# Kernel optimization log

Measured on AMD Instinct MI355X. Metric: run time of the kernel, lower is better.

The kernel has to match this reference:

```python
import jax, jax.numpy as jnp
import numpy as np
from math import sqrt

I = 1024  # input_size
H = 1024  # hidden_size
B = 4096  # batch


def setup_inputs() -> dict:
    key = jax.random.key(0)
    ks = jax.random.split(key, 12)
    a = 1.0 / sqrt(H)
    u = lambda k, shape: jax.random.uniform(k, shape, jnp.float32, -a, a)
    return {
        "x": jax.random.normal(ks[0], (B, I), jnp.float32),
        "hx": jax.random.normal(ks[1], (B, H), jnp.float32),
        "cx": jax.random.normal(ks[2], (B, H), jnp.float32),
        "weight_ih": u(ks[3], (4 * H, I)),
        "weight_hh": u(ks[4], (4 * H, H)),
        "bias_ih": u(ks[5], (4 * H,)),
        "bias_hh": u(ks[6], (4 * H,)),
        "W_peephole_i": u(ks[7], (H, H)),
        "W_peephole_f": u(ks[8], (H, H)),
        "W_peephole_o": u(ks[9], (H, H)),
    }


def reference(x, hx, cx, weight_ih, weight_hh, bias_ih, bias_hh,
              W_peephole_i, W_peephole_f, W_peephole_o):
    # gates: [B, 4H]
    gates = x @ weight_ih.T + bias_ih + hx @ weight_hh.T + bias_hh
    ingate, forgetgate, cellgate, outgate = jnp.split(gates, 4, axis=1)
    # F.linear(cx, W * eye) == cx * diag(W)  (diagonal peephole)
    ingate = jax.nn.sigmoid(ingate + cx * jnp.diagonal(W_peephole_i))
    forgetgate = jax.nn.sigmoid(forgetgate + cx * jnp.diagonal(W_peephole_f))
    cellgate = jnp.tanh(cellgate)
    cy = forgetgate * cx + ingate * cellgate
    # NOTE: original code reuses W_peephole_f for the output gate (faithful to source)
    outgate = jax.nn.sigmoid(outgate + cy * jnp.diagonal(W_peephole_f))
    hy = outgate * jnp.tanh(cy)
    return (hy, cy)
```

## Files before the change

kernel.cpp:

```cpp
#include <hip/hip_runtime.h>
#include <cstdint>


namespace {

constexpr int H   = 1024;
constexpr int K2  = 2048;
constexpr int BSZ = 4096;
constexpr size_t OUT_CY = (size_t)BSZ * H;

typedef __attribute__((ext_vector_type(8))) short bf16x8;
typedef __attribute__((ext_vector_type(4))) float f32x4;
typedef __attribute__((ext_vector_type(8))) unsigned short u16x8;

__device__ __forceinline__ unsigned short f2bf(float f) {
  union { float f; uint32_t u; } v; v.f = f;
  uint32_t u = v.u;
  u += 0x7FFFu + ((u >> 16) & 1u);
  return (unsigned short)(u >> 16);
}

__device__ __forceinline__ float sigm(float x) {
  return 1.0f / (1.0f + __expf(-x));
}
__device__ __forceinline__ float tanh_fast(float x) {
  return 1.0f - 2.0f / (1.0f + __expf(2.0f * x));
}

__device__ __forceinline__ void gload_lds16(const void* g, void* l) {
  __builtin_amdgcn_global_load_lds(
      (const __attribute__((address_space(1))) void*)g,
      (__attribute__((address_space(3))) void*)l, 16, 0, 0);
}

}

__global__ __launch_bounds__(256) void cast_kernel(
    const float* __restrict__ x, const float* __restrict__ hx,
    const float* __restrict__ wih, const float* __restrict__ whh,
    unsigned short* __restrict__ A, unsigned short* __restrict__ W) {
  int b = blockIdx.x;
  bool isW = b >= 4096;
  int t = (isW ? b - 4096 : b) * 256 + threadIdx.x;
  int idx = t * 8;
  int n = idx >> 11;
  int k = idx & 2047;
  const float* s0 = isW ? wih : x;
  const float* s1 = isW ? whh : hx;
  const float* src = (k < H) ? (s0 + (size_t)n * H + k)
                             : (s1 + (size_t)n * H + (k - H));
  float4 v0 = *(const float4*)src;
  float4 v1 = *(const float4*)(src + 4);
  u16x8 o;
  o[0] = f2bf(v0.x); o[1] = f2bf(v0.y); o[2] = f2bf(v0.z); o[3] = f2bf(v0.w);
  o[4] = f2bf(v1.x); o[5] = f2bf(v1.y); o[6] = f2bf(v1.z); o[7] = f2bf(v1.w);
  if (isW) {
    int g = n >> 10, hh = n & 1023;
    int np = ((hh >> 4) << 6) + (g << 4) + (hh & 15);
    *(u16x8*)(W + (size_t)np * K2 + k) = o;
  } else {
    *(u16x8*)(A + (size_t)idx) = o;
  }
}

__global__ __launch_bounds__(512, 2) void lstm_fused_gemm(
    const unsigned short* __restrict__ A,
    const unsigned short* __restrict__ W,
    const float* __restrict__ cx,
    const float* __restrict__ bias_ih, const float* __restrict__ bias_hh,
    const float* __restrict__ Wpi, const float* __restrict__ Wpf,
    float* __restrict__ out) {
  __shared__ __align__(16) unsigned short lds[2 * 32768];

  const int tid  = threadIdx.x;
  const int lane = tid & 63;
  const int wave = tid >> 6;
  const int wm   = wave >> 2;
  const int wn   = wave & 3;
  const int m0 = blockIdx.x * 256;
  const int w0 = blockIdx.y * 256;

  const int srow   = tid >> 3;
  const int schunk = ((tid & 7) ^ (srow & 7)) << 3;

  const int col  = lane & 15;
  const int quad = lane >> 4;

  const unsigned short* Asrc = A + (size_t)(m0 + srow) * K2 + schunk;
  const unsigned short* Wsrc = W + (size_t)(w0 + srow) * K2 + schunk;
  const int ldsdst = wave * 512;

  f32x4 acc[8][4];
#pragma unroll
  for (int i = 0; i < 8; ++i)
#pragma unroll
    for (int j = 0; j < 4; ++j)
      acc[i][j] = (f32x4){0.f, 0.f, 0.f, 0.f};

  auto stA = [&](int kt, int buf, int p) {
    gload_lds16(Asrc + (size_t)p * 64 * K2 + kt * 64,
                &lds[buf * 32768 + p * 4096 + ldsdst]);
  };
  auto stB = [&](int kt, int buf, int p) {
    gload_lds16(Wsrc + (size_t)p * 64 * K2 + kt * 64,
                &lds[buf * 32768 + 16384 + p * 4096 + ldsdst]);
  };

#pragma unroll
  for (int p = 0; p < 4; ++p) stA(0, 0, p);
#pragma unroll
  for (int p = 0; p < 4; ++p) stB(0, 0, p);
#pragma unroll
  for (int p = 0; p < 4; ++p) stA(1, 1, p);
#pragma unroll
  for (int p = 0; p < 4; ++p) stB(1, 1, p);
  asm volatile("s_waitcnt vmcnt(8)" ::: "memory");
  __builtin_amdgcn_sched_barrier(0);
  __builtin_amdgcn_s_barrier();

  const int aoff = (wm * 128 + col) * 64;
  const int boff = 16384 + (wn * 64 + col) * 64;
  const int kch0 = ((quad ^ (col & 7)) << 3);
  const int kch1 = (((4 + quad) ^ (col & 7)) << 3);

  for (int kt = 0; kt < 32; ++kt) {
    const int buf = kt & 1;
    const unsigned short* Lb = &lds[buf * 32768];
    const bool pf = (kt + 2 < 32);
    bf16x8 bfr[4][2];
#pragma unroll
    for (int q = 0; q < 4; ++q) {
      bf16x8 afr[2][2];
      if (q == 0) {
#pragma unroll
        for (int j = 0; j < 4; ++j) {
          bfr[j][0] = *(const bf16x8*)&Lb[boff + j * 1024 + kch0];
          bfr[j][1] = *(const bf16x8*)&Lb[boff + j * 1024 + kch1];
        }
      }
#pragma unroll
      for (int i2 = 0; i2 < 2; ++i2) {
        afr[i2][0] = *(const bf16x8*)&Lb[aoff + (2 * q + i2) * 1024 + kch0];
        afr[i2][1] = *(const bf16x8*)&Lb[aoff + (2 * q + i2) * 1024 + kch1];
      }
      if (q == 1 && pf) { stB(kt + 2, buf, 0); stB(kt + 2, buf, 1); }
      if (q == 2 && pf) { stB(kt + 2, buf, 2); stB(kt + 2, buf, 3); }
      if (q == 3 && pf) { stA(kt + 2, buf, 0); stA(kt + 2, buf, 2); }
      __builtin_amdgcn_s_barrier();
      asm volatile("s_waitcnt lgkmcnt(0)" ::: "memory");
      __builtin_amdgcn_sched_barrier(0);
      __builtin_amdgcn_s_setprio(1);
#pragma unroll
      for (int i2 = 0; i2 < 2; ++i2)
#pragma unroll
        for (int j = 0; j < 4; ++j) {
          acc[2 * q + i2][j] = __builtin_amdgcn_mfma_f32_16x16x32_bf16(
              afr[i2][0], bfr[j][0], acc[2 * q + i2][j], 0, 0, 0);
          acc[2 * q + i2][j] = __builtin_amdgcn_mfma_f32_16x16x32_bf16(
              afr[i2][1], bfr[j][1], acc[2 * q + i2][j], 0, 0, 0);
        }
      __builtin_amdgcn_s_setprio(0);
      __builtin_amdgcn_s_barrier();
    }
    if (pf) {
      stA(kt + 2, buf, 1); stA(kt + 2, buf, 3);
      asm volatile("s_waitcnt vmcnt(8)" ::: "memory");
    } else {
      asm volatile("s_waitcnt vmcnt(0)" ::: "memory");
    }
    __builtin_amdgcn_sched_barrier(0);
    __builtin_amdgcn_s_barrier();
  }

  const int h = blockIdx.y * 64 + wn * 16 + col;
  const float bi  = bias_ih[h]         + bias_hh[h];
  const float bf_ = bias_ih[H + h]     + bias_hh[H + h];
  const float bc  = bias_ih[2 * H + h] + bias_hh[2 * H + h];
  const float bo  = bias_ih[3 * H + h] + bias_hh[3 * H + h];
  const float di = Wpi[(size_t)h * (H + 1)];
  const float df = Wpf[(size_t)h * (H + 1)];
  const int mbase = m0 + wm * 128 + quad * 4;
#pragma unroll
  for (int i = 0; i < 8; ++i) {
#pragma unroll
    for (int r = 0; r < 4; ++r) {
      const int m = mbase + i * 16 + r;
      const float c  = cx[(size_t)m * H + h];
      const float ip = acc[i][0][r] + bi;
      const float fp = acc[i][1][r] + bf_;
      const float cp = acc[i][2][r] + bc;
      const float op = acc[i][3][r] + bo;
      const float ig = sigm(ip + c * di);
      const float fg = sigm(fp + c * df);
      const float cg = tanh_fast(cp);
      const float cy = fg * c + ig * cg;
      const float og = sigm(op + cy * df);
      const float hy = og * tanh_fast(cy);
      out[(size_t)m * H + h] = hy;
      out[OUT_CY + (size_t)m * H + h] = cy;
    }
  }
}

extern "C" void kernel_launch(void* const* d_in, const int* in_sizes, int n_in,
                              void* d_out, int out_size, void* d_ws, size_t ws_size,
                              hipStream_t stream) {
  const float* x   = (const float*)d_in[0];
  const float* hx  = (const float*)d_in[1];
  const float* cx  = (const float*)d_in[2];
  const float* wih = (const float*)d_in[3];
  const float* whh = (const float*)d_in[4];
  const float* bih = (const float*)d_in[5];
  const float* bhh = (const float*)d_in[6];
  const float* wpi = (const float*)d_in[7];
  const float* wpf = (const float*)d_in[8];
  float* out = (float*)d_out;

  unsigned short* Abf = (unsigned short*)d_ws;
  unsigned short* Wbf = Abf + (size_t)BSZ * K2;

  cast_kernel<<<8192, 256, 0, stream>>>(x, hx, wih, whh, Abf, Wbf);

  dim3 grid(BSZ / 256, (4 * H) / 256);
  lstm_fused_gemm<<<grid, 512, 0, stream>>>(Abf, Wbf, cx, bih, bhh, wpi, wpf, out);
}
```

Baseline: 206.7 us.

## Swizzle block-to-XCD mapping, use inline-asm LDS reads, reorder MFMAs, unroll k-loop

Remaps the 2D block grid so that blocks landing on the same XCD (round-robin by linear block id) share A/W tiles, improving L2 reuse. LDS fragment reads become inline-asm ds_read_b128 with precomputed byte addresses. The MFMA chain is reordered so consecutive MFMAs target different accumulators, avoiding back-to-back dependencies, and the k-loop is unrolled by 2. The asm volatile reads hide dependencies from the compiler and may weaken its scheduling of waitcnts, which is risky.

```diff
diff --git a/kernel.cpp b/kernel.cpp
--- a/kernel.cpp
+++ b/kernel.cpp
@@ -31,6 +31,12 @@
   __builtin_amdgcn_global_load_lds(
       (const __attribute__((address_space(1))) void*)g,
       (__attribute__((address_space(3))) void*)l, 16, 0, 0);
+}
+
+__device__ __forceinline__ bf16x8 dsr_b128(unsigned addr) {
+  bf16x8 r;
+  asm volatile("ds_read_b128 %0, %1" : "=v"(r) : "v"(addr));
+  return r;
 }
 
 }
@@ -77,8 +83,13 @@
   const int wave = tid >> 6;
   const int wm   = wave >> 2;
   const int wn   = wave & 3;
-  const int m0 = blockIdx.x * 256;
-  const int w0 = blockIdx.y * 256;
+
+  const int b   = blockIdx.y * 16 + blockIdx.x;
+  const int xcd = b & 7, idx = b >> 3;
+  const int bx  = (xcd & 3) * 4 + (idx & 3);
+  const int by  = (xcd >> 2) * 8 + (idx >> 2);
+  const int m0 = bx * 256;
+  const int w0 = by * 256;
 
   const int srow   = tid >> 3;
   const int schunk = ((tid & 7) ^ (srow & 7)) << 3;
@@ -118,14 +129,16 @@
   __builtin_amdgcn_sched_barrier(0);
   __builtin_amdgcn_s_barrier();
 
-  const int aoff = (wm * 128 + col) * 64;
-  const int boff = 16384 + (wn * 64 + col) * 64;
-  const int kch0 = ((quad ^ (col & 7)) << 3);
-  const int kch1 = (((4 + quad) ^ (col & 7)) << 3);
-
+  const unsigned lds0 = (unsigned)(size_t)(__attribute__((address_space(3))) char*)lds;
+  const unsigned abase = lds0 + (unsigned)((wm * 128 + col) * 128);
+  const unsigned bbase = lds0 + 32768u + (unsigned)((wn * 64 + col) * 128);
+  const unsigned kch0 = ((quad ^ (col & 7)) << 4);
+  const unsigned kch1 = (((4 + quad) ^ (col & 7)) << 4);
+
+#pragma unroll 2
   for (int kt = 0; kt < 32; ++kt) {
     const int buf = kt & 1;
-    const unsigned short* Lb = &lds[buf * 32768];
+    const unsigned boffs = (unsigned)(buf * 65536);
     const bool pf = (kt + 2 < 32);
     bf16x8 bfr[4][2];
 #pragma unroll
@@ -134,14 +147,14 @@
       if (q == 0) {
 #pragma unroll
         for (int j = 0; j < 4; ++j) {
-          bfr[j][0] = *(const bf16x8*)&Lb[boff + j * 1024 + kch0];
-          bfr[j][1] = *(const bf16x8*)&Lb[boff + j * 1024 + kch1];
+          bfr[j][0] = dsr_b128(bbase + boffs + j * 2048 + kch0);
+          bfr[j][1] = dsr_b128(bbase + boffs + j * 2048 + kch1);
         }
       }
 #pragma unroll
       for (int i2 = 0; i2 < 2; ++i2) {
-        afr[i2][0] = *(const bf16x8*)&Lb[aoff + (2 * q + i2) * 1024 + kch0];
-        afr[i2][1] = *(const bf16x8*)&Lb[aoff + (2 * q + i2) * 1024 + kch1];
+        afr[i2][0] = dsr_b128(abase + boffs + (2 * q + i2) * 2048 + kch0);
+        afr[i2][1] = dsr_b128(abase + boffs + (2 * q + i2) * 2048 + kch1);
       }
       if (q == 1 && pf) { stB(kt + 2, buf, 0); stB(kt + 2, buf, 1); }
       if (q == 2 && pf) { stB(kt + 2, buf, 2); stB(kt + 2, buf, 3); }
@@ -153,12 +166,15 @@
 #pragma unroll
       for (int i2 = 0; i2 < 2; ++i2)
 #pragma unroll
-        for (int j = 0; j < 4; ++j) {
+        for (int j = 0; j < 4; ++j)
           acc[2 * q + i2][j] = __builtin_amdgcn_mfma_f32_16x16x32_bf16(
               afr[i2][0], bfr[j][0], acc[2 * q + i2][j], 0, 0, 0);
+#pragma unroll
+      for (int i2 = 0; i2 < 2; ++i2)
+#pragma unroll
+        for (int j = 0; j < 4; ++j)
           acc[2 * q + i2][j] = __builtin_amdgcn_mfma_f32_16x16x32_bf16(
               afr[i2][1], bfr[j][1], acc[2 * q + i2][j], 0, 0, 0);
-        }
       __builtin_amdgcn_s_setprio(0);
       __builtin_amdgcn_s_barrier();
     }
@@ -172,7 +188,7 @@
     __builtin_amdgcn_s_barrier();
   }
 
-  const int h = blockIdx.y * 64 + wn * 16 + col;
+  const int h = by * 64 + wn * 16 + col;
   const float bi  = bias_ih[h]         + bias_hh[h];
   const float bf_ = bias_ih[H + h]     + bias_hh[H + h];
   const float bc  = bias_ih[2 * H + h] + bias_hh[2 * H + h];
```

New measurement: 203.1 us. Within noise of the previous version (-1.8%).
